# Performance work log

Measured on AMD Instinct MI355X. Metric: run time of the kernel, lower is better.

Reference implementation:

```python
import math
import jax, jax.numpy as jnp
import numpy as np

B, D, T, C, H = 4096, 1024, 768, 16, 4
CURV = 0.05
EPS = 1e-8
ASINH_MAX = float(np.arcsinh(2.0 ** 15))

# ---------- Poincare ball ops (hyptorch.pmath) ----------

def artanh(x):
    x = jnp.clip(x, -1 + 1e-5, 1 - 1e-5)
    return 0.5 * (jnp.log1p(x) - jnp.log1p(-x))

def p_logmap0(y, c):
    sc = c ** 0.5
    n = jnp.clip(jnp.linalg.norm(y, axis=-1, keepdims=True), 1e-15, None)
    return y / (n * sc) * artanh(sc * n)

def p_expmap0(u, c):
    sc = c ** 0.5
    n = jnp.clip(jnp.linalg.norm(u, axis=-1, keepdims=True), 1e-15, None)
    return jnp.tanh(sc * n) * u / (sc * n)

def p_project(x, c):
    maxn = (1 - 4e-3) / c ** 0.5  # float32 eps in hyptorch
    n = jnp.clip(jnp.linalg.norm(x, axis=-1, keepdims=True), 1e-15, None)
    return jnp.where(n > maxn, x / n * maxn, x)

# ---------- Lorentz ops (MERU-style L module) ----------

def l_expmap0(x, c):
    rc = (c ** 0.5) * jnp.linalg.norm(x, axis=-1, keepdims=True)
    si = jnp.clip(rc, EPS, ASINH_MAX)
    return jnp.sinh(si) * x / jnp.clip(rc, EPS, None)

def l_logmap0(x, c):
    rc = (c ** 0.5) * jnp.linalg.norm(x, axis=-1, keepdims=True)
    return jnp.arcsinh(rc) * x / jnp.clip(rc, EPS, None)

def oxy_angle(x, y, c):
    xt = jnp.sqrt(1.0 / c + jnp.sum(x * x, -1))
    yt = jnp.sqrt(1.0 / c + jnp.sum(y * y, -1))
    c_xyl = c * (jnp.sum(x * y, -1) - xt * yt)
    num = yt + c_xyl * xt
    den = jnp.sqrt(jnp.clip(c_xyl ** 2 - 1.0, EPS, None))
    acos_in = num / (jnp.linalg.norm(x, axis=-1) * den + EPS)
    return jnp.arccos(jnp.clip(acos_in, -1 + EPS, 1 - EPS))

def half_aperture(x, c, min_radius=0.1):
    asin_in = 2.0 * min_radius / (jnp.linalg.norm(x, axis=-1) * c ** 0.5 + EPS)
    return jnp.arcsin(jnp.clip(asin_in, -1 + EPS, 1 - EPS))

# ---------- small building blocks ----------

def layernorm(x, w, b, eps=1e-5):
    mu = jnp.mean(x, -1, keepdims=True)
    var = jnp.mean((x - mu) ** 2, -1, keepdims=True)
    return (x - mu) * jax.lax.rsqrt(var + eps) * w + b

def mha(x, w_in, b_in, w_out, b_out):
    # x: (B, S=4, D), torch nn.MultiheadAttention, batch_first, 4 heads
    Bq, S, Dm = x.shape
    hd = Dm // H
    qkv = x @ w_in.T + b_in
    q, k, v = jnp.split(qkv, 3, axis=-1)
    rs = lambda t: t.reshape(Bq, S, H, hd).transpose(0, 2, 1, 3)
    q, k, v = rs(q), rs(k), rs(v)
    a = jax.nn.softmax(jnp.einsum('bhqd,bhkd->bhqk', q, k) / math.sqrt(hd), axis=-1)
    o = jnp.einsum('bhqk,bhkd->bhqd', a, v).transpose(0, 2, 1, 3).reshape(Bq, S, Dm)
    return o @ w_out.T + b_out

def mobius_add_batch(x, y, c):
    # x: (C, D) (the -p points), y: (B, D) -> (C, B, D)
    xy = x @ y.T                               # (C, B)
    x2 = jnp.sum(x * x, -1, keepdims=True)     # (C, 1)
    y2 = jnp.sum(y * y, -1)                    # (B,)
    num = (1 + 2 * c * xy + c * y2[None, :])[..., None] * x[:, None, :] \
        + (1 - c * x2)[..., None] * y[None, :, :]
    den = 1 + 2 * c * xy + c * c * x2 * y2[None, :]
    return num / (den[..., None] + 1e-5)

def hyperbolic_mlr(x, a, p, c):
    sc = c ** 0.5
    p_p = p_expmap0(p, c)                      # (C, D)
    conf = 1 - c * jnp.sum(p_p ** 2, -1, keepdims=True)
    a_p = a * conf                             # (C, D)
    lam = 2.0 / (1 - c * jnp.sum(p_p ** 2, -1))
    a_norm = jnp.linalg.norm(a_p, axis=-1)     # (C,)
    kk = lam * a_norm / sc
    mob = mobius_add_batch(-p_p, x, c)         # (C, B, D)
    num = 2 * sc * jnp.einsum('cbd,cd->cb', mob, a_p)
    den = a_norm[:, None] * (1 - c * jnp.sum(mob ** 2, -1))
    return (kk[:, None] * jnp.arcsinh(num / den)).T  # (B, C)

def hyp_loss_fn(order_hyp, family_hyp, order, family, mask,
                to_w, to_b, tf_w, tf_b):
    order_feats = l_expmap0(order @ to_w.T + to_b, CURV)
    order_loss = jnp.mean(jax.nn.relu(
        oxy_angle(order_feats, family_hyp, CURV) - half_aperture(order_feats, CURV)))
    fam_feats = l_expmap0(family @ tf_w.T + tf_b, CURV)
    fpen = jax.nn.relu(
        oxy_angle(fam_feats, order_hyp, CURV) - half_aperture(fam_feats, CURV))
    m = mask.astype(order.dtype)
    cnt = jnp.sum(m)
    family_loss = jnp.where(cnt > 0, jnp.sum(fpen * m) / jnp.clip(cnt, 1.0, None), 0.0)
    return order_loss + family_loss


def setup_inputs() -> dict:
    key = jax.random.key(0)
    ks = jax.random.split(key, 20)
    g = lambda k, s, sc: jax.random.normal(k, s, jnp.float32) * sc
    inp = {
        # Poincare-ball points: scale down so sqrt(c)*||x|| << 1
        'order_hyp': g(ks[0], (B, D), 0.02),
        'family_hyp': g(ks[1], (B, D), 0.02),
        'order_euc': g(ks[2], (B, D), 1.0),
        'family_euc': g(ks[3], (B, D), 1.0),
        'order': g(ks[4], (B, T), 1.0),
        'family': g(ks[5], (B, T), 1.0),
        'mask': jax.random.randint(ks[6], (B,), 0, 2, jnp.int32),
        # MultiheadAttention params
        'in_proj_w': g(ks[7], (3 * D, D), D ** -0.5),
        'in_proj_b': jnp.zeros((3 * D,), jnp.float32),
        'out_proj_w': g(ks[8], (D, D), D ** -0.5),
        'out_proj_b': jnp.zeros((D,), jnp.float32),
        # LayerNorm
        'ln_w': jnp.ones((D,), jnp.float32),
        'ln_b': jnp.zeros((D,), jnp.float32),
        # text projections
        'to_w': g(ks[9], (D, T), T ** -0.5),
        'to_b': jnp.zeros((D,), jnp.float32),
        'tf_w': g(ks[10], (D, T), T ** -0.5),
        'tf_b': jnp.zeros((D,), jnp.float32),
        # HyperbolicMLR params
        'mlr_a': g(ks[11], (C, D), 0.02),
        'mlr_p': g(ks[12], (C, D), 0.02),
    }
    return inp


def reference(order_hyp, family_hyp, order_euc, family_euc, order, family, mask,
              in_proj_w, in_proj_b, out_proj_w, out_proj_b, ln_w, ln_b,
              to_w, to_b, tf_w, tf_b, mlr_a, mlr_p):
    # FromPoincare (logmap0 on the ball)
    fh_e = p_logmap0(family_hyp, CURV)
    oh_e = p_logmap0(order_hyp, CURV)
    gf = jnp.stack([oh_e, fh_e, order_euc, family_euc], axis=1)  # (B, 4, D)
    attn = mha(gf, in_proj_w, in_proj_b, out_proj_w, out_proj_b)
    gf = layernorm(gf + attn, ln_w, ln_b)
    oh, fh, oeu, feu = gf[:, 0], gf[:, 1], gf[:, 2], gf[:, 3]
    fh = l_expmap0(fh, CURV)
    oh = l_expmap0(oh, CURV)
    hyp_loss = hyp_loss_fn(oh, fh, order, family, mask, to_w, to_b, tf_w, tf_b)
    oh_out = l_logmap0(oh, CURV)
    hyp_pt = p_project(p_expmap0(oh_out, CURV), CURV)  # ToPoincare(riemannian=False)
    logits = hyperbolic_mlr(hyp_pt, mlr_a, mlr_p, CURV)
    return (logits, hyp_loss, oh, fh, oeu, feu)
```

## Files before the change

kernel.cpp:

```cpp
#include <hip/hip_runtime.h>
#include <stdint.h>

#define BB    4096
#define DD    1024
#define TT    768
#define CC    16
#define HH    4
#define SS    4
#define HD    256
#define M1    (BB*SS)
#define CURVF 0.05f
#define SCF   0.22360679774997896f
#define EPSF  1e-8f
#define ASINH_MAXF 11.090354888959125f

#define OFF_LOGITS 0ull
#define OFF_LOSS   65536ull
#define OFF_OH     65537ull
#define OFF_FH     (65537ull + 4194304ull)
#define OFF_OEU    (65537ull + 2ull*4194304ull)
#define OFF_FEU    (65537ull + 3ull*4194304ull)

typedef __attribute__((ext_vector_type(8))) short bf16x8;
typedef __attribute__((ext_vector_type(4))) float f32x4;

__device__ __forceinline__ float bf2f(unsigned short h) {
  union { unsigned int u; float f; } v; v.u = ((unsigned int)h) << 16; return v.f;
}
__device__ __forceinline__ unsigned short f2bf(float f) {
  union { float f; unsigned int u; } v; v.f = f;
  unsigned int u = v.u;
  return (unsigned short)((u + 0x7FFFu + ((u >> 16) & 1u)) >> 16);
}
__device__ __forceinline__ ushort4 f2bf4(float4 v) {
  ushort4 o; o.x = f2bf(v.x); o.y = f2bf(v.y); o.z = f2bf(v.z); o.w = f2bf(v.w);
  return o;
}
__device__ __forceinline__ float wsum(float v) {
#pragma unroll
  for (int o = 32; o > 0; o >>= 1) v += __shfl_xor(v, o, 64);
  return v;
}
__device__ __forceinline__ float block_sum(float v, float* red) {
  v = wsum(v);
  int lane = threadIdx.x & 63, wv = threadIdx.x >> 6;
  __syncthreads();
  if (lane == 0) red[wv] = v;
  __syncthreads();
  return red[0] + red[1] + red[2] + red[3];
}
__device__ __forceinline__ float artanh_clip(float x) {
  x = fminf(fmaxf(x, -1.0f + 1e-5f), 1.0f - 1e-5f);
  return 0.5f * (log1pf(x) - log1pf(-x));
}

typedef __attribute__((address_space(1))) const void gas_void;
typedef __attribute__((address_space(3))) void las_void;
__device__ __forceinline__ void gld16(void* l, const void* g) {
  __builtin_amdgcn_global_load_lds((gas_void*)g, (las_void*)l, 16, 0, 0);
}

struct Cvt6 {
  const float4* src[6];
  unsigned short* dst[6];
  unsigned int end4[6];
};
__global__ __launch_bounds__(256) void k_cvt6(Cvt6 c, unsigned int total4) {
  unsigned int i = blockIdx.x * 256 + threadIdx.x;
  if (i >= total4) return;
#pragma unroll
  for (int j = 0; j < 6; j++) {
    if (i < c.end4[j]) {
      unsigned int k = i - (j ? c.end4[j - 1] : 0u);
      ((ushort4*)c.dst[j])[k] = f2bf4(c.src[j][k]);
      return;
    }
  }
}

__global__ __launch_bounds__(256) void k_prep_gf(const float* __restrict__ ohyp,
    const float* __restrict__ fhyp, const float* __restrict__ oeuc,
    const float* __restrict__ feuc, unsigned short* __restrict__ gf) {
  __shared__ float red[4];
  int b = blockIdx.x;
  int t = threadIdx.x;
  size_t base4 = (size_t)b * (DD / 4);
  float4 xo = ((const float4*)ohyp)[base4 + t];
  float4 xf = ((const float4*)fhyp)[base4 + t];
  float so = xo.x * xo.x + xo.y * xo.y + xo.z * xo.z + xo.w * xo.w;
  float sf = xf.x * xf.x + xf.y * xf.y + xf.z * xf.z + xf.w * xf.w;
  float no2 = block_sum(so, red);
  float nf2 = block_sum(sf, red);
  float no = fmaxf(sqrtf(no2), 1e-15f);
  float nf = fmaxf(sqrtf(nf2), 1e-15f);
  float fo = artanh_clip(SCF * no) / (no * SCF);
  float ff = artanh_clip(SCF * nf) / (nf * SCF);
  size_t g0 = (size_t)b * 4 * (DD / 4);
  float4 e2 = ((const float4*)oeuc)[base4 + t];
  float4 e3 = ((const float4*)feuc)[base4 + t];
  float4 y0 = {xo.x * fo, xo.y * fo, xo.z * fo, xo.w * fo};
  float4 y1 = {xf.x * ff, xf.y * ff, xf.z * ff, xf.w * ff};
  ((ushort4*)gf)[g0 + t]              = f2bf4(y0);
  ((ushort4*)gf)[g0 + DD / 4 + t]     = f2bf4(y1);
  ((ushort4*)gf)[g0 + 2 * DD / 4 + t] = f2bf4(e2);
  ((ushort4*)gf)[g0 + 3 * DD / 4 + t] = f2bf4(e3);
}

template <int OUT_BF16>
__device__ __forceinline__ void gemm_body(
    unsigned short* As, unsigned short* Bs,
    const unsigned short* __restrict__ A, const unsigned short* __restrict__ Bm,
    const float* __restrict__ bias, void* __restrict__ Cv,
    int M, int N, int K, int bx, int by) {
  const int tid = threadIdx.x;
  const int lane = tid & 63;
  const int wv = tid >> 6;
  const long tileM = (long)by * 128;
  const long tileN = (long)bx * 128;

  f32x4 acc[4][4];
#pragma unroll
  for (int i = 0; i < 4; i++)
#pragma unroll
    for (int j = 0; j < 4; j++) acc[i][j] = (f32x4){0.f, 0.f, 0.f, 0.f};

  const int srow = wv * 16 + (lane >> 2);
  const int lc = (lane & 3) ^ ((srow >> 1) & 3);
  const unsigned short* Ag = A + (tileM + srow) * (long)K + lc * 8;
  const unsigned short* Bg = Bm + (tileN + srow) * (long)K + lc * 8;
  unsigned short* Asl = As + srow * 32 + (lane & 3) * 8;
  unsigned short* Bsl = Bs + srow * 32 + (lane & 3) * 8;

  const int fr = lane & 15;
  const int rkey = (fr >> 1) & 3;
  const int fko2 = (((lane >> 4) ^ rkey)) * 8;
  const int wr = (wv >> 1) * 64;
  const int wc = (wv & 1) * 64;

  for (int k0 = 0; k0 < K; k0 += 32) {
    gld16(Asl, Ag + k0);
    gld16(Asl + 64 * 32, Ag + (long)64 * K + k0);
    gld16(Bsl, Bg + k0);
    gld16(Bsl + 64 * 32, Bg + (long)64 * K + k0);
    __syncthreads();
    bf16x8 af[4], bfr[4];
#pragma unroll
    for (int i = 0; i < 4; i++)
      af[i] = *(const bf16x8*)(As + (wr + i * 16 + fr) * 32 + fko2);
#pragma unroll
    for (int j = 0; j < 4; j++)
      bfr[j] = *(const bf16x8*)(Bs + (wc + j * 16 + fr) * 32 + fko2);
#pragma unroll
    for (int i = 0; i < 4; i++)
#pragma unroll
      for (int j = 0; j < 4; j++)
        acc[i][j] = __builtin_amdgcn_mfma_f32_16x16x32_bf16(af[i], bfr[j], acc[i][j], 0, 0, 0);
    __syncthreads();
  }

  const int er = (lane >> 4) * 4;
  const int ec = lane & 15;
#pragma unroll
  for (int i = 0; i < 4; i++) {
#pragma unroll
    for (int j = 0; j < 4; j++) {
      long col = tileN + wc + j * 16 + ec;
      float bv = bias ? bias[col] : 0.f;
#pragma unroll
      for (int r = 0; r < 4; r++) {
        long row = tileM + wr + i * 16 + er + r;
        float v = acc[i][j][r] + bv;
        if (OUT_BF16) ((unsigned short*)Cv)[row * (long)N + col] = f2bf(v);
        else          ((float*)Cv)[row * (long)N + col] = v;
      }
    }
  }
}

template <int OUT_BF16>
__global__ __launch_bounds__(256) void k_gemm_bt(
    const unsigned short* __restrict__ A, const unsigned short* __restrict__ Bm,
    const float* __restrict__ bias, void* __restrict__ Cv, int M, int N, int K) {
  __shared__ unsigned short As[128 * 32];
  __shared__ unsigned short Bs[128 * 32];
  gemm_body<OUT_BF16>(As, Bs, A, Bm, bias, Cv, M, N, K, blockIdx.x, blockIdx.y);
}

__global__ __launch_bounds__(256) void k_gemm_loss(
    const unsigned short* __restrict__ A0, const unsigned short* __restrict__ B0,
    const float* __restrict__ b0, float* __restrict__ C0,
    const unsigned short* __restrict__ A1, const unsigned short* __restrict__ B1,
    const float* __restrict__ b1, float* __restrict__ C1, int M, int N, int K) {
  __shared__ unsigned short As[128 * 32];
  __shared__ unsigned short Bs[128 * 32];
  if (blockIdx.z == 0)
    gemm_body<0>(As, Bs, A0, B0, b0, C0, M, N, K, blockIdx.x, blockIdx.y);
  else
    gemm_body<0>(As, Bs, A1, B1, b1, C1, M, N, K, blockIdx.x, blockIdx.y);
}

__global__ __launch_bounds__(256) void k_attn(const unsigned short* __restrict__ qkv,
                                              unsigned short* __restrict__ o) {
  int b = blockIdx.x;
  int h = blockIdx.y;
  int lane = threadIdx.x & 63;
  int qi = threadIdx.x >> 6;
  const unsigned short* base = qkv + (size_t)b * 4 * 3072 + h * HD;
  int d = lane * 4;
  float qv[4], kv[4][4], vv[4][4];
  {
    ushort4 q4 = *(const ushort4*)(base + (size_t)qi * 3072 + d);
    qv[0] = bf2f(q4.x); qv[1] = bf2f(q4.y); qv[2] = bf2f(q4.z); qv[3] = bf2f(q4.w);
  }
#pragma unroll
  for (int j = 0; j < 4; j++) {
    ushort4 k4 = *(const ushort4*)(base + (size_t)j * 3072 + 1024 + d);
    ushort4 v4 = *(const ushort4*)(base + (size_t)j * 3072 + 2048 + d);
    kv[j][0] = bf2f(k4.x); kv[j][1] = bf2f(k4.y); kv[j][2] = bf2f(k4.z); kv[j][3] = bf2f(k4.w);
    vv[j][0] = bf2f(v4.x); vv[j][1] = bf2f(v4.y); vv[j][2] = bf2f(v4.z); vv[j][3] = bf2f(v4.w);
  }
  float sc_[4];
#pragma unroll
  for (int j = 0; j < 4; j++) {
    float p = 0.f;
#pragma unroll
    for (int t = 0; t < 4; t++) p += qv[t] * kv[j][t];
    sc_[j] = wsum(p) * (1.0f / 16.0f);
  }
  float mx = fmaxf(fmaxf(sc_[0], sc_[1]), fmaxf(sc_[2], sc_[3]));
  float e[4], den = 0.f;
#pragma unroll
  for (int j = 0; j < 4; j++) { e[j] = expf(sc_[j] - mx); den += e[j]; }
  float inv = 1.0f / den;
  float4 ov = {0.f, 0.f, 0.f, 0.f};
#pragma unroll
  for (int j = 0; j < 4; j++) {
    float w = e[j] * inv;
    ov.x += w * vv[j][0]; ov.y += w * vv[j][1];
    ov.z += w * vv[j][2]; ov.w += w * vv[j][3];
  }
  *(ushort4*)(o + (size_t)(b * 4 + qi) * DD + h * HD + d) = f2bf4(ov);
}

__global__ __launch_bounds__(256) void k_ln_split(const unsigned short* __restrict__ gf,
    const unsigned short* __restrict__ attn, const float* __restrict__ lnw,
    const float* __restrict__ lnb, float* __restrict__ dout) {
  __shared__ float red[4];
  int r = blockIdx.x;
  int b = r >> 2, s = r & 3;
  int t = threadIdx.x;
  size_t base4 = (size_t)r * (DD / 4);
  ushort4 g4 = ((const ushort4*)gf)[base4 + t];
  ushort4 a4 = ((const ushort4*)attn)[base4 + t];
  float x[4] = {bf2f(g4.x) + bf2f(a4.x), bf2f(g4.y) + bf2f(a4.y),
                bf2f(g4.z) + bf2f(a4.z), bf2f(g4.w) + bf2f(a4.w)};
  float sum = x[0] + x[1] + x[2] + x[3];
  float sq = x[0] * x[0] + x[1] * x[1] + x[2] * x[2] + x[3] * x[3];
  sum = block_sum(sum, red);
  sq  = block_sum(sq, red);
  float mu = sum * (1.0f / (float)DD);
  float var = sq * (1.0f / (float)DD) - mu * mu;
  float inv = rsqrtf(var + 1e-5f);
  float4 w4 = ((const float4*)lnw)[t];
  float4 b4 = ((const float4*)lnb)[t];
  float y[4];
  y[0] = (x[0] - mu) * inv * w4.x + b4.x;
  y[1] = (x[1] - mu) * inv * w4.y + b4.y;
  y[2] = (x[2] - mu) * inv * w4.z + b4.z;
  y[3] = (x[3] - mu) * inv * w4.w + b4.w;
  float fmul = 1.0f;
  if (s < 2) {
    float n2 = y[0] * y[0] + y[1] * y[1] + y[2] * y[2] + y[3] * y[3];
    n2 = block_sum(n2, red);
    float rc = SCF * sqrtf(n2);
    float si = fminf(fmaxf(rc, EPSF), ASINH_MAXF);
    fmul = sinhf(si) / fmaxf(rc, EPSF);
  }
  size_t offs = (s == 0) ? OFF_OH : (s == 1) ? OFF_FH : (s == 2) ? OFF_OEU : OFF_FEU;
  float4* outp = (float4*)(dout + offs + (size_t)b * DD);
  float4 o4 = {y[0] * fmul, y[1] * fmul, y[2] * fmul, y[3] * fmul};
  outp[t] = o4;
}

__global__ __launch_bounds__(256) void k_oxy(const float* __restrict__ raw0,
    const float* __restrict__ y0, const float* __restrict__ raw1,
    const float* __restrict__ y1, float* __restrict__ pens) {
  __shared__ float red[4];
  int b = blockIdx.x;
  int which = blockIdx.y;
  const float* raw = which ? raw1 : raw0;
  const float* yr  = which ? y1 : y0;
  size_t base = (size_t)b * DD;
  float sxx = 0.f, sxy = 0.f, syy = 0.f;
#pragma unroll
  for (int k = 0; k < 4; k++) {
    int d = threadIdx.x + 256 * k;
    float xv = raw[base + d];
    float yv = yr[base + d];
    sxx += xv * xv; sxy += xv * yv; syy += yv * yv;
  }
  sxx = block_sum(sxx, red);
  sxy = block_sum(sxy, red);
  syy = block_sum(syy, red);
  if (threadIdx.x == 0) {
    float nraw = sqrtf(sxx);
    float rc = SCF * nraw;
    float si = fminf(fmaxf(rc, EPSF), ASINH_MAXF);
    float f = sinhf(si) / fmaxf(rc, EPSF);
    float x2 = f * f * sxx;
    float xy = f * sxy;
    float y2 = syy;
    float nx = f * nraw;
    float xt = sqrtf(1.0f / CURVF + x2);
    float yt = sqrtf(1.0f / CURVF + y2);
    float c_xyl = CURVF * (xy - xt * yt);
    float num = yt + c_xyl * xt;
    float den = sqrtf(fmaxf(c_xyl * c_xyl - 1.0f, EPSF));
    float ai = num / (nx * den + EPSF);
    ai = fminf(fmaxf(ai, -1.0f + EPSF), 1.0f - EPSF);
    float ang = acosf(ai);
    float asi = 0.2f / (nx * SCF + EPSF);
    asi = fminf(fmaxf(asi, -1.0f + EPSF), 1.0f - EPSF);
    float ap = asinf(asi);
    pens[(size_t)which * BB + b] = fmaxf(ang - ap, 0.0f);
  }
}

__global__ __launch_bounds__(256) void k_finalize_loss(const float* __restrict__ pens,
    const int* __restrict__ mask, float* __restrict__ dout) {
  __shared__ float red[4];
  float s0 = 0.f, s1 = 0.f, cnt = 0.f;
  for (int i = threadIdx.x; i < BB; i += 256) {
    s0 += pens[i];
    float m = (float)mask[i];
    s1 += pens[BB + i] * m;
    cnt += m;
  }
  s0 = block_sum(s0, red);
  s1 = block_sum(s1, red);
  cnt = block_sum(cnt, red);
  if (threadIdx.x == 0) {
    float order_loss = s0 / (float)BB;
    float fam = (cnt > 0.f) ? s1 / fmaxf(cnt, 1.0f) : 0.0f;
    dout[OFF_LOSS] = order_loss + fam;
  }
}

__global__ __launch_bounds__(256) void k_mlr_prep(const float* __restrict__ a,
    const float* __restrict__ p, float* __restrict__ p_p, float* __restrict__ a_p,
    float* __restrict__ cs) {
  __shared__ float red[4];
  int c = blockIdx.x;
  int t = threadIdx.x;
  size_t base4 = (size_t)c * (DD / 4);
  float4 pv = ((const float4*)p)[base4 + t];
  float4 av = ((const float4*)a)[base4 + t];
  float sp = pv.x * pv.x + pv.y * pv.y + pv.z * pv.z + pv.w * pv.w;
  float sa = av.x * av.x + av.y * av.y + av.z * av.z + av.w * av.w;
  float spa = pv.x * av.x + pv.y * av.y + pv.z * av.z + pv.w * av.w;
  sp = block_sum(sp, red); sa = block_sum(sa, red); spa = block_sum(spa, red);
  float n = fmaxf(sqrtf(sp), 1e-15f);
  float f = tanhf(SCF * n) / (SCF * n);
  float x2 = f * f * sp;
  float conf = 1.0f - CURVF * x2;
  float a_norm = fabsf(conf) * sqrtf(sa);
  float lam = 2.0f / (1.0f - CURVF * x2);
  float kk = lam * a_norm / SCF;
  float xa = -f * conf * spa;
  float4 pp = {pv.x * f, pv.y * f, pv.z * f, pv.w * f};
  float4 ap = {av.x * conf, av.y * conf, av.z * conf, av.w * conf};
  ((float4*)p_p)[base4 + t] = pp;
  ((float4*)a_p)[base4 + t] = ap;
  if (threadIdx.x == 0) {
    cs[c * 5 + 0] = x2; cs[c * 5 + 1] = conf; cs[c * 5 + 2] = a_norm;
    cs[c * 5 + 3] = kk; cs[c * 5 + 4] = xa;
  }
}

__global__ __launch_bounds__(256) void k_mlr_logits(const float* __restrict__ oh,
    const float* __restrict__ p_p, const float* __restrict__ a_p,
    const float* __restrict__ cs, float* __restrict__ logits) {
  __shared__ float row[DD];
  __shared__ float dots[CC][2];
  __shared__ float s_n2;
  int b = blockIdx.x;
  int lane = threadIdx.x & 63, wv = threadIdx.x >> 6;
  const float* src = oh + (size_t)b * DD;
#pragma unroll
  for (int k = 0; k < 4; k++)
    row[threadIdx.x + 256 * k] = src[threadIdx.x + 256 * k];
  __syncthreads();
  if (wv == 0) {
    float n2p = 0.f;
#pragma unroll
    for (int k = 0; k < 4; k++) {
      float4 v = ((const float4*)row)[lane + 64 * k];
      n2p += v.x * v.x + v.y * v.y + v.z * v.z + v.w * v.w;
    }
    n2p = wsum(n2p);
    if (lane == 0) s_n2 = n2p;
  }
#pragma unroll
  for (int ccc = 0; ccc < 4; ccc++) {
    int c = wv * 4 + ccc;
    const float4* pp4 = (const float4*)(p_p + (size_t)c * DD);
    const float4* ap4 = (const float4*)(a_p + (size_t)c * DD);
    float dp = 0.f, da = 0.f;
#pragma unroll
    for (int k = 0; k < 4; k++) {
      int d4 = lane + 64 * k;
      float4 v = ((const float4*)row)[d4];
      float4 p4 = pp4[d4];
      float4 a4 = ap4[d4];
      dp += p4.x * v.x + p4.y * v.y + p4.z * v.z + p4.w * v.w;
      da += a4.x * v.x + a4.y * v.y + a4.z * v.z + a4.w * v.w;
    }
    dp = wsum(dp); da = wsum(da);
    if (lane == 0) { dots[c][0] = dp; dots[c][1] = da; }
  }
  __syncthreads();
  if (threadIdx.x < CC) {
    int c = threadIdx.x;
    float n2 = s_n2;
    float n1 = sqrtf(n2);
    float rc = SCF * n1;
    float g = asinhf(rc) / fmaxf(rc, EPSF);
    float nu = fmaxf(n1 * g, 1e-15f);
    float fac = tanhf(SCF * nu) / (SCF * nu);
    float s = g * fac;
    float ny = fmaxf(n1 * s, 1e-15f);
    float maxn = (1.0f - 0.004f) / SCF;
    if (ny > maxn) s *= maxn / ny;
    float y2 = s * s * n2;
    float py = s * dots[c][0];
    float ay = s * dots[c][1];
    float x2 = cs[c * 5 + 0], conf = cs[c * 5 + 1], a_norm = cs[c * 5 + 2];
    float kk = cs[c * 5 + 3], xa = cs[c * 5 + 4];
    float xy = -py;
    float A = 1.f + 2.f * CURVF * xy + CURVF * y2;
    float den0 = 1.f + 2.f * CURVF * xy + CURVF * CURVF * x2 * y2;
    float d = den0 + 1e-5f;
    float num = 2.f * SCF * (A * xa + conf * ay) / d;
    float mob2 = (A * A * x2 + 2.f * A * conf * xy + conf * conf * y2) / (d * d);
    float denl = a_norm * (1.f - CURVF * mob2);
    logits[(size_t)b * CC + c] = kk * asinhf(num / denl);
  }
}

extern "C" void kernel_launch(void* const* d_in, const int* in_sizes, int n_in,
                              void* d_out, int out_size, void* d_ws, size_t ws_size,
                              hipStream_t stream) {
  const float* order_hyp  = (const float*)d_in[0];
  const float* family_hyp = (const float*)d_in[1];
  const float* order_euc  = (const float*)d_in[2];
  const float* family_euc = (const float*)d_in[3];
  const float* order      = (const float*)d_in[4];
  const float* family     = (const float*)d_in[5];
  const int*   mask       = (const int*)d_in[6];
  const float* in_proj_w  = (const float*)d_in[7];
  const float* in_proj_b  = (const float*)d_in[8];
  const float* out_proj_w = (const float*)d_in[9];
  const float* out_proj_b = (const float*)d_in[10];
  const float* ln_w       = (const float*)d_in[11];
  const float* ln_b       = (const float*)d_in[12];
  const float* to_w       = (const float*)d_in[13];
  const float* to_b       = (const float*)d_in[14];
  const float* tf_w       = (const float*)d_in[15];
  const float* tf_b       = (const float*)d_in[16];
  const float* mlr_a      = (const float*)d_in[17];
  const float* mlr_p      = (const float*)d_in[18];
  float* dout = (float*)d_out;

  char* w = (char*)d_ws;
  size_t off = 0;
  auto take = [&](size_t n) { char* p = w + off; off += (n + 255) & ~(size_t)255; return p; };
  unsigned short* gf_bf   = (unsigned short*)take((size_t)M1 * DD * 2);
  unsigned short* region2 = (unsigned short*)take((size_t)M1 * 3 * DD * 2);
  unsigned short* o_bf    = (unsigned short*)take((size_t)M1 * DD * 2);
  unsigned short* win_bf  = (unsigned short*)take((size_t)3 * DD * DD * 2);
  unsigned short* wout_bf = (unsigned short*)take((size_t)DD * DD * 2);
  unsigned short* tow_bf  = (unsigned short*)take((size_t)DD * TT * 2);
  unsigned short* tfw_bf  = (unsigned short*)take((size_t)DD * TT * 2);
  unsigned short* ord_bf  = (unsigned short*)take((size_t)BB * TT * 2);
  unsigned short* fam_bf  = (unsigned short*)take((size_t)BB * TT * 2);
  float* p_p   = (float*)take((size_t)CC * DD * 4);
  float* a_p   = (float*)take((size_t)CC * DD * 4);
  float* cs    = (float*)take(CC * 5 * 4);
  float* pens  = (float*)take((size_t)2 * BB * 4);

  unsigned short* qkv     = region2;
  unsigned short* attn_bf = region2;
  float* ofeat = (float*)((char*)region2 + 33554432);
  float* ffeat = (float*)((char*)region2 + 50331648);

  Cvt6 cv;
  cv.src[0] = (const float4*)in_proj_w;  cv.dst[0] = win_bf;
  cv.src[1] = (const float4*)out_proj_w; cv.dst[1] = wout_bf;
  cv.src[2] = (const float4*)to_w;       cv.dst[2] = tow_bf;
  cv.src[3] = (const float4*)tf_w;       cv.dst[3] = tfw_bf;
  cv.src[4] = (const float4*)order;      cv.dst[4] = ord_bf;
  cv.src[5] = (const float4*)family;     cv.dst[5] = fam_bf;
  unsigned int n4[6] = {3u * DD * DD / 4, DD * DD / 4, DD * TT / 4, DD * TT / 4,
                        BB * TT / 4, BB * TT / 4};
  unsigned int acc4 = 0;
  for (int j = 0; j < 6; j++) { acc4 += n4[j]; cv.end4[j] = acc4; }
  k_cvt6<<<(acc4 + 255) / 256, 256, 0, stream>>>(cv, acc4);

  k_prep_gf<<<BB, 256, 0, stream>>>(order_hyp, family_hyp, order_euc, family_euc, gf_bf);

  k_gemm_bt<1><<<dim3(3 * DD / 128, M1 / 128), 256, 0, stream>>>(
      gf_bf, win_bf, in_proj_b, qkv, M1, 3 * DD, DD);

  k_attn<<<dim3(BB, HH), 256, 0, stream>>>(qkv, o_bf);

  k_gemm_bt<1><<<dim3(DD / 128, M1 / 128), 256, 0, stream>>>(
      o_bf, wout_bf, out_proj_b, attn_bf, M1, DD, DD);

  k_ln_split<<<M1, 256, 0, stream>>>(gf_bf, attn_bf, ln_w, ln_b, dout);

  k_gemm_loss<<<dim3(DD / 128, BB / 128, 2), 256, 0, stream>>>(
      ord_bf, tow_bf, to_b, ofeat, fam_bf, tfw_bf, tf_b, ffeat, BB, DD, TT);

  k_oxy<<<dim3(BB, 2), 256, 0, stream>>>(ofeat, dout + OFF_FH, ffeat, dout + OFF_OH, pens);
  k_finalize_loss<<<1, 256, 0, stream>>>(pens, mask, dout);

  k_mlr_prep<<<CC, 256, 0, stream>>>(mlr_a, mlr_p, p_p, a_p, cs);
  k_mlr_logits<<<BB, 256, 0, stream>>>(dout + OFF_OH, p_p, a_p, cs, dout + OFF_LOGITS);

  (void)in_sizes; (void)n_in; (void)out_size; (void)ws_size;
}
```

Baseline: 518.3 us.

## Use 256x256-tile pipelined MFMA GEMM for attention in/out projections

Replaces the 128x128 tiled GEMM used for the MHA input and output projections with a new 512-thread kernel that computes 256x256 tiles. It uses a 4-stage LDS ring fed by direct global-to-LDS loads with explicit vmcnt waits, raises wave priority around MFMA bursts, and remaps workgroup IDs into XCD-aware order. The goal is more data reuse per tile and better overlap of loads with matrix math. In exchange it needs 128KB of LDS per block and 128 accumulator registers per thread, which limits occupancy and makes the tail wave coarser.

```diff
diff --git a/kernel.cpp b/kernel.cpp
--- a/kernel.cpp
+++ b/kernel.cpp
@@ -59,6 +59,8 @@
 __device__ __forceinline__ void gld16(void* l, const void* g) {
   __builtin_amdgcn_global_load_lds((gas_void*)g, (las_void*)l, 16, 0, 0);
 }
+
+#define VMCNT(n) asm volatile("s_waitcnt vmcnt(" #n ")" ::: "memory")
 
 struct Cvt6 {
   const float4* src[6];
@@ -107,6 +109,115 @@
 }
 
 template <int OUT_BF16>
+__global__ __launch_bounds__(512) void k_gemm256(
+    const unsigned short* __restrict__ A, const unsigned short* __restrict__ Bm,
+    const float* __restrict__ bias, void* __restrict__ Cv,
+    int N, int K, int nx) {
+  __shared__ unsigned short lds[4][2][8192];
+  const int nwg = gridDim.x;
+  const int rid = blockIdx.x;
+  const int wg = (rid & 7) * (nwg >> 3) + (rid >> 3);
+  const int bx = wg % nx;
+  const int by = wg / nx;
+  const long tileM = (long)by * 256;
+  const long tileN = (long)bx * 256;
+  const int tid = threadIdx.x;
+  const int lane = tid & 63;
+  const int wv = tid >> 6;
+  const int wr = wv >> 2;
+  const int wc = wv & 3;
+  const int NT = K >> 5;
+
+  f32x4 acc[8][4];
+#pragma unroll
+  for (int i = 0; i < 8; i++)
+#pragma unroll
+    for (int j = 0; j < 4; j++) acc[i][j] = (f32x4){0.f, 0.f, 0.f, 0.f};
+
+  const int srow = tid >> 2;
+  const unsigned short* Ag = A + (tileM + srow) * (long)K + (tid & 3) * 8;
+  const unsigned short* Bg = Bm + (tileN + srow) * (long)K + (tid & 3) * 8;
+
+  auto stageA = [&](int t) {
+    int b = t & 3;
+    const unsigned short* s = Ag + t * 32;
+    gld16(&lds[b][0][tid * 8], s);
+    gld16(&lds[b][0][4096 + tid * 8], s + (long)128 * K);
+  };
+  auto stageB = [&](int t) {
+    int b = t & 3;
+    const unsigned short* s = Bg + t * 32;
+    gld16(&lds[b][1][tid * 8], s);
+    gld16(&lds[b][1][4096 + tid * 8], s + (long)128 * K);
+  };
+
+  stageA(0); stageB(0);
+  stageA(1); stageB(1);
+  stageA(2); stageB(2);
+  VMCNT(8);
+  __builtin_amdgcn_s_barrier();
+  asm volatile("" ::: "memory");
+
+  const int fr = lane & 15;
+  const int hi = lane >> 4;
+
+  for (int t = 0; t < NT; ++t) {
+    const unsigned short* Ab = &lds[t & 3][0][0];
+    const unsigned short* Bb = &lds[t & 3][1][0];
+    bf16x8 af[4], bfr[4];
+#pragma unroll
+    for (int j = 0; j < 4; j++)
+      bfr[j] = *(const bf16x8*)(Bb + (wc * 64 + j * 16 + fr) * 32 + hi * 8);
+#pragma unroll
+    for (int i = 0; i < 4; i++)
+      af[i] = *(const bf16x8*)(Ab + (wr * 128 + i * 16 + fr) * 32 + hi * 8);
+    if (t + 3 < NT) stageA(t + 3);
+    __builtin_amdgcn_s_setprio(1);
+#pragma unroll
+    for (int i = 0; i < 4; i++)
+#pragma unroll
+      for (int j = 0; j < 4; j++)
+        acc[i][j] = __builtin_amdgcn_mfma_f32_16x16x32_bf16(af[i], bfr[j], acc[i][j], 0, 0, 0);
+    __builtin_amdgcn_s_setprio(0);
+#pragma unroll
+    for (int i = 0; i < 4; i++)
+      af[i] = *(const bf16x8*)(Ab + (wr * 128 + (i + 4) * 16 + fr) * 32 + hi * 8);
+    if (t + 3 < NT) stageB(t + 3);
+    __builtin_amdgcn_s_setprio(1);
+#pragma unroll
+    for (int i = 0; i < 4; i++)
+#pragma unroll
+      for (int j = 0; j < 4; j++)
+        acc[i + 4][j] = __builtin_amdgcn_mfma_f32_16x16x32_bf16(af[i], bfr[j], acc[i + 4][j], 0, 0, 0);
+    __builtin_amdgcn_s_setprio(0);
+    if (t + 1 < NT) {
+      if (t + 3 < NT)      VMCNT(8);
+      else if (t + 2 < NT) VMCNT(4);
+      else                 VMCNT(0);
+      __builtin_amdgcn_s_barrier();
+      asm volatile("" ::: "memory");
+    }
+  }
+
+  const int er = hi * 4;
+#pragma unroll
+  for (int i = 0; i < 8; i++) {
+#pragma unroll
+    for (int j = 0; j < 4; j++) {
+      long col = tileN + wc * 64 + j * 16 + fr;
+      float bv = bias ? bias[col] : 0.f;
+#pragma unroll
+      for (int r = 0; r < 4; r++) {
+        long row = tileM + wr * 128 + i * 16 + er + r;
+        float v = acc[i][j][r] + bv;
+        if (OUT_BF16) ((unsigned short*)Cv)[row * (long)N + col] = f2bf(v);
+        else          ((float*)Cv)[row * (long)N + col] = v;
+      }
+    }
+  }
+}
+
+template <int OUT_BF16>
 __device__ __forceinline__ void gemm_body(
     unsigned short* As, unsigned short* Bs,
     const unsigned short* __restrict__ A, const unsigned short* __restrict__ Bm,
@@ -175,15 +286,6 @@
       }
     }
   }
-}
-
-template <int OUT_BF16>
-__global__ __launch_bounds__(256) void k_gemm_bt(
-    const unsigned short* __restrict__ A, const unsigned short* __restrict__ Bm,
-    const float* __restrict__ bias, void* __restrict__ Cv, int M, int N, int K) {
-  __shared__ unsigned short As[128 * 32];
-  __shared__ unsigned short Bs[128 * 32];
-  gemm_body<OUT_BF16>(As, Bs, A, Bm, bias, Cv, M, N, K, blockIdx.x, blockIdx.y);
 }
 
 __global__ __launch_bounds__(256) void k_gemm_loss(
@@ -508,13 +610,19 @@
 
   k_prep_gf<<<BB, 256, 0, stream>>>(order_hyp, family_hyp, order_euc, family_euc, gf_bf);
 
-  k_gemm_bt<1><<<dim3(3 * DD / 128, M1 / 128), 256, 0, stream>>>(
-      gf_bf, win_bf, in_proj_b, qkv, M1, 3 * DD, DD);
+  {
+    int nx = 3 * DD / 256, ny = M1 / 256;
+    k_gemm256<1><<<nx * ny, 512, 0, stream>>>(
+        gf_bf, win_bf, in_proj_b, qkv, 3 * DD, DD, nx);
+  }
 
   k_attn<<<dim3(BB, HH), 256, 0, stream>>>(qkv, o_bf);
 
-  k_gemm_bt<1><<<dim3(DD / 128, M1 / 128), 256, 0, stream>>>(
-      o_bf, wout_bf, out_proj_b, attn_bf, M1, DD, DD);
+  {
+    int nx = DD / 256, ny = M1 / 256;
+    k_gemm256<1><<<nx * ny, 512, 0, stream>>>(
+        o_bf, wout_bf, out_proj_b, attn_bf, DD, DD, nx);
+  }
 
   k_ln_split<<<M1, 256, 0, stream>>>(gf_bf, attn_bf, ln_w, ln_b, dout);
 
```

After: 472.1 us. 8.9% less time.

## Replace 128x128 GEMM with 256x256 double-buffered 8-wave MFMA kernel

Applied to the files above, without the earlier changes.

Replaces the in-projection and out-projection GEMMs with a new kernel that uses 256x256 output tiles, 512 threads and BK=64. Shared-memory loads are XOR-swizzled and double-buffered with direct global-to-LDS loads. The kernel interleaves A/B sub-tile loads with MFMA groups under explicit waitcnt, barriers and setprio, and remaps workgroups for L2 locality. The aim is higher arithmetic intensity and overlap of memory with MFMA in the two largest GEMMs. The cost is heavy register and LDS use and many barriers per K step.

```diff
diff --git a/kernel.cpp b/kernel.cpp
--- a/kernel.cpp
+++ b/kernel.cpp
@@ -59,6 +59,10 @@
 __device__ __forceinline__ void gld16(void* l, const void* g) {
   __builtin_amdgcn_global_load_lds((gas_void*)g, (las_void*)l, 16, 0, 0);
 }
+
+#define VMCNT(n) asm volatile("s_waitcnt vmcnt(" #n ")" ::: "memory")
+#define BARRIER() do { asm volatile("" ::: "memory"); __builtin_amdgcn_s_barrier(); asm volatile("" ::: "memory"); } while (0)
+#define LGKM0() do { asm volatile("s_waitcnt lgkmcnt(0)" ::: "memory"); __builtin_amdgcn_sched_barrier(0); } while (0)
 
 struct Cvt6 {
   const float4* src[6];
@@ -107,6 +111,140 @@
 }
 
 template <int OUT_BF16>
+__global__ __launch_bounds__(512, 2) void k_gemm256(
+    const unsigned short* __restrict__ A, const unsigned short* __restrict__ Bm,
+    const float* __restrict__ bias, void* __restrict__ Cv,
+    int N, int K, int nx) {
+  __shared__ unsigned short As[2 * 2 * 128 * 64];
+  __shared__ unsigned short Bs[2 * 2 * 128 * 64];
+  const int nwg = gridDim.x;
+  const int rid = blockIdx.x;
+  const int wg = (rid & 7) * (nwg >> 3) + (rid >> 3);
+  const int bx = wg % nx;
+  const int by = wg / nx;
+  const long tileM = (long)by * 256;
+  const long tileN = (long)bx * 256;
+  const int tid = threadIdx.x;
+  const int lane = tid & 63;
+  const int wv = tid >> 6;
+  const int wr = wv >> 2;
+  const int wc = wv & 3;
+  const int NT = K >> 6;
+
+  f32x4 acc[8][4];
+#pragma unroll
+  for (int i = 0; i < 8; i++)
+#pragma unroll
+    for (int j = 0; j < 4; j++) acc[i][j] = (f32x4){0.f, 0.f, 0.f, 0.f};
+
+  const int srow = tid >> 3;
+  const int sc = (tid & 7) ^ (srow & 7);
+  const unsigned short* Ag = A + (tileM + srow) * (long)K + sc * 8;
+  const unsigned short* Bg = Bm + (tileN + srow) * (long)K + sc * 8;
+
+#define STAGE_A(T_) do { \
+    unsigned short* d_ = As + ((T_) & 1) * 16384; \
+    const unsigned short* g_ = Ag + (long)(T_) * 64; \
+    gld16(d_ + tid * 8,          g_); \
+    gld16(d_ + 4096 + tid * 8,   g_ + (long)64 * K); \
+    gld16(d_ + 8192 + tid * 8,   g_ + (long)128 * K); \
+    gld16(d_ + 12288 + tid * 8,  g_ + (long)192 * K); } while (0)
+#define STAGE_BLO(T_) do { \
+    unsigned short* d_ = Bs + ((T_) & 1) * 16384; \
+    const unsigned short* g_ = Bg + (long)(T_) * 64; \
+    gld16(d_ + tid * 8,          g_); \
+    gld16(d_ + 4096 + tid * 8,   g_ + (long)64 * K); } while (0)
+#define STAGE_BHI(T_) do { \
+    unsigned short* d_ = Bs + ((T_) & 1) * 16384 + 8192; \
+    const unsigned short* g_ = Bg + (long)(T_) * 64 + (long)128 * K; \
+    gld16(d_ + tid * 8,          g_); \
+    gld16(d_ + 4096 + tid * 8,   g_ + (long)64 * K); } while (0)
+
+  const int fr = lane & 15;
+  const int hi = lane >> 4;
+  const int fx = fr & 7;
+  const unsigned short* ArdBase = As + wr * 8192 + fr * 64;
+  const unsigned short* BrdBase = Bs + (wc >> 1) * 8192 + (wc & 1) * 4096 + fr * 64;
+
+#define LDA8(dst_, p_, ihsel_) do { \
+    const unsigned short* b_ = ArdBase + (p_) * 16384 + (ihsel_) * 4096; \
+    _Pragma("unroll") for (int i2_ = 0; i2_ < 4; i2_++) \
+    _Pragma("unroll") for (int s_ = 0; s_ < 2; s_++) \
+      dst_[i2_][s_] = *(const bf16x8*)(b_ + i2_ * 1024 + ((s_ * 4 + hi) ^ fx) * 8); } while (0)
+#define LDB4(dst_, p_, jhsel_) do { \
+    const unsigned short* b_ = BrdBase + (p_) * 16384 + (jhsel_) * 2048; \
+    _Pragma("unroll") for (int j2_ = 0; j2_ < 2; j2_++) \
+    _Pragma("unroll") for (int s_ = 0; s_ < 2; s_++) \
+      dst_[j2_][s_] = *(const bf16x8*)(b_ + j2_ * 1024 + ((s_ * 4 + hi) ^ fx) * 8); } while (0)
+#define MFMA16(ihsel_, jhsel_, a_, b_) do { \
+    __builtin_amdgcn_s_setprio(1); \
+    _Pragma("unroll") for (int i2_ = 0; i2_ < 4; i2_++) \
+    _Pragma("unroll") for (int j2_ = 0; j2_ < 2; j2_++) { \
+      acc[(ihsel_)*4 + i2_][(jhsel_)*2 + j2_] = __builtin_amdgcn_mfma_f32_16x16x32_bf16( \
+          a_[i2_][0], b_[j2_][0], acc[(ihsel_)*4 + i2_][(jhsel_)*2 + j2_], 0, 0, 0); \
+      acc[(ihsel_)*4 + i2_][(jhsel_)*2 + j2_] = __builtin_amdgcn_mfma_f32_16x16x32_bf16( \
+          a_[i2_][1], b_[j2_][1], acc[(ihsel_)*4 + i2_][(jhsel_)*2 + j2_], 0, 0, 0); \
+    } \
+    __builtin_amdgcn_s_setprio(0); } while (0)
+
+  STAGE_A(0); STAGE_BLO(0); STAGE_BHI(0); STAGE_A(1);
+  VMCNT(4);
+  BARRIER();
+
+  bf16x8 a_[4][2], b0_[2][2], b1_[2][2];
+  for (int T = 0; T < NT; ++T) {
+    const int p = T & 1;
+    LDA8(a_, p, 0);
+    LDB4(b0_, p, 0);
+    if (T + 1 < NT) STAGE_BLO(T + 1);
+    BARRIER();
+    LGKM0();
+    MFMA16(0, 0, a_, b0_);
+    BARRIER();
+    LDB4(b1_, p, 1);
+    if (T + 1 < NT) STAGE_BHI(T + 1);
+    BARRIER();
+    LGKM0();
+    MFMA16(0, 1, a_, b1_);
+    BARRIER();
+    LDA8(a_, p, 1);
+    BARRIER();
+    LGKM0();
+    MFMA16(1, 1, a_, b1_);
+    BARRIER();
+    if (T + 2 < NT) { STAGE_A(T + 2); VMCNT(4); }
+    else            { VMCNT(0); }
+    BARRIER();
+    MFMA16(1, 0, a_, b0_);
+    BARRIER();
+  }
+
+#undef STAGE_A
+#undef STAGE_BLO
+#undef STAGE_BHI
+#undef LDA8
+#undef LDB4
+#undef MFMA16
+
+  const int er = hi * 4;
+#pragma unroll
+  for (int i = 0; i < 8; i++) {
+#pragma unroll
+    for (int j = 0; j < 4; j++) {
+      long col = tileN + wc * 64 + j * 16 + fr;
+      float bv = bias ? bias[col] : 0.f;
+#pragma unroll
+      for (int r = 0; r < 4; r++) {
+        long row = tileM + wr * 128 + i * 16 + er + r;
+        float v = acc[i][j][r] + bv;
+        if (OUT_BF16) ((unsigned short*)Cv)[row * (long)N + col] = f2bf(v);
+        else          ((float*)Cv)[row * (long)N + col] = v;
+      }
+    }
+  }
+}
+
+template <int OUT_BF16>
 __device__ __forceinline__ void gemm_body(
     unsigned short* As, unsigned short* Bs,
     const unsigned short* __restrict__ A, const unsigned short* __restrict__ Bm,
@@ -175,15 +313,6 @@
       }
     }
   }
-}
-
-template <int OUT_BF16>
-__global__ __launch_bounds__(256) void k_gemm_bt(
-    const unsigned short* __restrict__ A, const unsigned short* __restrict__ Bm,
-    const float* __restrict__ bias, void* __restrict__ Cv, int M, int N, int K) {
-  __shared__ unsigned short As[128 * 32];
-  __shared__ unsigned short Bs[128 * 32];
-  gemm_body<OUT_BF16>(As, Bs, A, Bm, bias, Cv, M, N, K, blockIdx.x, blockIdx.y);
 }
 
 __global__ __launch_bounds__(256) void k_gemm_loss(
@@ -508,13 +637,19 @@
 
   k_prep_gf<<<BB, 256, 0, stream>>>(order_hyp, family_hyp, order_euc, family_euc, gf_bf);
 
-  k_gemm_bt<1><<<dim3(3 * DD / 128, M1 / 128), 256, 0, stream>>>(
-      gf_bf, win_bf, in_proj_b, qkv, M1, 3 * DD, DD);
+  {
+    int nx = 3 * DD / 256, ny = M1 / 256;
+    k_gemm256<1><<<nx * ny, 512, 0, stream>>>(
+        gf_bf, win_bf, in_proj_b, qkv, 3 * DD, DD, nx);
+  }
 
   k_attn<<<dim3(BB, HH), 256, 0, stream>>>(qkv, o_bf);
 
-  k_gemm_bt<1><<<dim3(DD / 128, M1 / 128), 256, 0, stream>>>(
-      o_bf, wout_bf, out_proj_b, attn_bf, M1, DD, DD);
+  {
+    int nx = DD / 256, ny = M1 / 256;
+    k_gemm256<1><<<nx * ny, 512, 0, stream>>>(
+        o_bf, wout_bf, out_proj_b, attn_bf, DD, DD, nx);
+  }
 
   k_ln_split<<<M1, 256, 0, stream>>>(gf_bf, attn_bf, ln_w, ln_b, dout);
 
```

After: 470.9 us. -9.2%, faster.
